# Kernel optimization log

Hardware: AMD Instinct MI355X
Metric: run time of the kernel (lower is better)

The kernel has to match this reference:

```python
import jax, jax.numpy as jnp
import numpy as np

N_NODES = 50000
N_EDGES = 800000
D = 128


def setup_inputs() -> dict:
    key = jax.random.key(0)
    ks = jax.random.split(key, 8)
    h = jax.random.normal(ks[0], (N_NODES, D), dtype=jnp.float32)
    src = jax.random.randint(ks[1], (N_EDGES,), 0, N_NODES, dtype=jnp.int64)
    dst = jax.random.randint(ks[2], (N_EDGES,), 0, N_NODES, dtype=jnp.int64)
    # Glorot-ish init for the three GraphConv weights
    scale = 1.0 / np.sqrt(D)
    W0 = jax.random.normal(ks[3], (D, D), dtype=jnp.float32) * scale
    W1 = jax.random.normal(ks[4], (D, D), dtype=jnp.float32) * scale
    W2 = jax.random.normal(ks[5], (D, D), dtype=jnp.float32) * scale
    b0 = jnp.zeros((D,), dtype=jnp.float32)
    b1 = jnp.zeros((D,), dtype=jnp.float32)
    b2 = jnp.zeros((D,), dtype=jnp.float32)
    return {"h": h, "src": src, "dst": dst, "W0": W0, "b0": b0,
            "W1": W1, "b1": b1, "W2": W2, "b2": b2}


def _graph_conv(x, src, dst, W, b, n_nodes):
    """DGL GraphConv, norm='both', activation=ReLU.
    in_feats == out_feats -> aggregate first, then matmul W."""
    ones = jnp.ones_like(src, dtype=x.dtype)
    out_deg = jnp.clip(jax.ops.segment_sum(ones, src, num_segments=n_nodes), 1.0)
    in_deg = jnp.clip(jax.ops.segment_sum(ones, dst, num_segments=n_nodes), 1.0)
    x = x * (out_deg ** -0.5)[:, None]          # src-side normalization
    m = jax.ops.segment_sum(x[src], dst, num_segments=n_nodes)  # sparse aggregation
    m = m * (in_deg ** -0.5)[:, None]           # dst-side normalization
    return jax.nn.relu(m @ W + b)


def reference(h, src, dst, W0, b0, W1, b1, W2, b2):
    n = h.shape[0]
    h = _graph_conv(h, src, dst, W0, b0, n)
    h = _graph_conv(h, src, dst, W1, b1, n)
    h = _graph_conv(h, src, dst, W2, b2, n)
    return h
```

## Files before the change

### kernel.cpp

```cpp
#include <hip/hip_runtime.h>

#define N_NODES 50000
#define N_EDGES 800000
#define D 128
#define CAP 48
#define MS_STRIDE 132
#define QNODES 12500
#define QWORDS (QNODES / 4)
#define HISTB 1024
#define EPB (N_EDGES / 256)
#define HWORDS (N_NODES / 4)
#define FILLB ((N_EDGES + 255) / 256)
#define REDB ((HWORDS + 255) / 256)

typedef __attribute__((ext_vector_type(4))) float f32x4;
typedef __attribute__((ext_vector_type(8))) short s16x8;

__device__ inline unsigned short f32_to_bf16_rtne(float f) {
    union { float f; unsigned u; } c; c.f = f;
    unsigned u = c.u;
    u += 0x7FFF + ((u >> 16) & 1);
    return (unsigned short)(u >> 16);
}
__device__ inline float bf16_to_f32(unsigned short h) {
    union { unsigned u; float f; } c; c.u = ((unsigned)h) << 16;
    return c.f;
}
__device__ inline unsigned pack_bf2(float a, float b) {
    return (unsigned)f32_to_bf16_rtne(a) | ((unsigned)f32_to_bf16_rtne(b) << 16);
}
__device__ inline void unpack_bf2(unsigned u, float& a, float& b) {
    union { unsigned u; float f; } c0, c1;
    c0.u = u << 16; c1.u = u & 0xFFFF0000u;
    a = c0.f; b = c1.f;
}
__device__ inline void acc_uint4(uint4 v, float* a) {
    float f0, f1;
    unpack_bf2(v.x, f0, f1); a[0] += f0; a[1] += f1;
    unpack_bf2(v.y, f0, f1); a[2] += f0; a[3] += f1;
    unpack_bf2(v.z, f0, f1); a[4] += f0; a[5] += f1;
    unpack_bf2(v.w, f0, f1); a[6] += f0; a[7] += f1;
}


__global__ __launch_bounds__(256) void build_all(const int* __restrict__ src,
                                                 const int* __restrict__ dst,
                                                 int* __restrict__ cursor,
                                                 unsigned* __restrict__ partial,
                                                 int* __restrict__ slots) {
    __shared__ unsigned hist[QWORDS];
    int b = blockIdx.x;
    if (b < HISTB) {
        int q = b >> 8, p = b & 255;
        int n0 = q * QNODES;
        for (int i = threadIdx.x; i < QWORDS; i += 256) hist[i] = 0;
        __syncthreads();
        int e0 = p * EPB;
        for (int i = threadIdx.x; i < EPB; i += 256) {
            int s = src[e0 + i];
            unsigned r = (unsigned)(s - n0);
            if (r < (unsigned)QNODES) atomicAdd(&hist[r >> 2], 1u << ((r & 3) * 8));
        }
        __syncthreads();
        unsigned* dstp = partial + (size_t)b * QWORDS;
        for (int i = threadIdx.x; i < QWORDS; i += 256) dstp[i] = hist[i];
    } else {
        int e = (b - HISTB) * 256 + threadIdx.x;
        if (e < N_EDGES) {
            int d = dst[e], s = src[e];
            int pos = atomicAdd(&cursor[d], 1);
            if (pos < CAP) slots[d * CAP + pos] = s;
        }
    }
}


__global__ __launch_bounds__(256) void mid_reduce_pack(const unsigned* __restrict__ partial,
                                                       float* __restrict__ s_out,
                                                       const float* __restrict__ W0,
                                                       const float* __restrict__ W1,
                                                       const float* __restrict__ W2,
                                                       s16x8* __restrict__ wpk) {
    int blk = blockIdx.x;
    if (blk < REDB) {
        int w = blk * 256 + threadIdx.x;
        if (w >= HWORDS) return;
        int q = w / QWORDS, wq = w - q * QWORDS;
        const unsigned* base = partial + (size_t)(q * 256) * QWORDS + wq;
        int c0 = 0, c1 = 0, c2 = 0, c3 = 0;
        for (int p = 0; p < 256; p++) {
            unsigned v = base[(size_t)p * QWORDS];
            c0 += v & 255; c1 += (v >> 8) & 255; c2 += (v >> 16) & 255; c3 += v >> 24;
        }
        float4 so;
        so.x = rsqrtf(fmaxf((float)c0, 1.0f));
        so.y = rsqrtf(fmaxf((float)c1, 1.0f));
        so.z = rsqrtf(fmaxf((float)c2, 1.0f));
        so.w = rsqrtf(fmaxf((float)c3, 1.0f));
        ((float4*)s_out)[w] = so;
    } else {
        int wid = (blk - REDB) * 4 + (threadIdx.x >> 6);
        if (wid >= 96) return;
        int lane = threadIdx.x & 63;
        int layer = wid / 32, rem = wid % 32;
        int ct = rem >> 2, ks = rem & 3;
        const float* W = (layer == 0) ? W0 : (layer == 1) ? W1 : W2;
        int col = ct * 16 + (lane & 15);
        int k0  = ks * 32 + (lane >> 4) * 8;
        s16x8 hi, lo;
#pragma unroll
        for (int j = 0; j < 8; j++) {
            float w = W[(k0 + j) * D + col];
            unsigned short h = f32_to_bf16_rtne(w);
            hi[j] = (short)h;
            lo[j] = (short)f32_to_bf16_rtne(w - bf16_to_f32(h));
        }
        int idx = layer * 4096 + (ct * 4 + ks) * 64 + lane;
        wpk[idx]        = hi;
        wpk[idx + 2048] = lo;
    }
}


__global__ __launch_bounds__(256) void hconv(const float4* __restrict__ h,
                                             const float* __restrict__ s_out,
                                             uint2* __restrict__ hbA,
                                             uint2* __restrict__ hbB) {
    int gid = blockIdx.x * 256 + threadIdx.x;
    const int total = N_NODES * 32;
    if (gid < total) {
        float so = s_out[gid >> 5];
        float4 v = h[gid];
        hbA[gid] = make_uint2(pack_bf2(so * v.x, so * v.y), pack_bf2(so * v.z, so * v.w));
    } else if (gid < total + 32) {
        hbA[total + (gid - total)] = make_uint2(0u, 0u);
    } else if (gid < total + 64) {
        hbB[total + (gid - total - 32)] = make_uint2(0u, 0u);
    }
}


__global__ __launch_bounds__(256) void fused_layer(const uint4* __restrict__ x,
                                                   const int* __restrict__ slots,
                                                   const int* __restrict__ deg,
                                                   const s16x8* __restrict__ wpk,
                                                   const float* __restrict__ bias,
                                                   const float* __restrict__ s_out,
                                                   float* __restrict__ outf,
                                                   unsigned short* __restrict__ outb) {
    __shared__ float mS[16 * MS_STRIDE];
    int tid = threadIdx.x;
    int row0 = blockIdx.x * 16;

    {
        int nloc = tid >> 4;
        int l    = tid & 15;
        int node = row0 + nloc;
        int dgraw = deg[node];
        int dg = min(dgraw, CAP);
        int base = node * CAP;
        int idx0 = (l      < dg) ? slots[base + l]      : N_NODES;
        int idx1 = (16 + l < dg) ? slots[base + 16 + l] : N_NODES;
        int idx2 = (32 + l < dg) ? slots[base + 32 + l] : N_NODES;

        float a[8];
#pragma unroll
        for (int j = 0; j < 8; j++) a[j] = 0.f;

        int nr = (dg + 7) >> 3;
        for (int r = 0; r < nr; r++) {
            int c = r >> 1;
            int v = (c == 0) ? idx0 : ((c == 1) ? idx1 : idx2);
            int k = (r & 1) * 8;
            int s0 = __shfl(v, k + 0, 16), s1 = __shfl(v, k + 1, 16);
            int s2 = __shfl(v, k + 2, 16), s3 = __shfl(v, k + 3, 16);
            int s4 = __shfl(v, k + 4, 16), s5 = __shfl(v, k + 5, 16);
            int s6 = __shfl(v, k + 6, 16), s7 = __shfl(v, k + 7, 16);
            uint4 g0 = x[s0 * 16 + l];
            uint4 g1 = x[s1 * 16 + l];
            uint4 g2 = x[s2 * 16 + l];
            uint4 g3 = x[s3 * 16 + l];
            uint4 g4 = x[s4 * 16 + l];
            uint4 g5 = x[s5 * 16 + l];
            uint4 g6 = x[s6 * 16 + l];
            uint4 g7 = x[s7 * 16 + l];
            acc_uint4(g0, a); acc_uint4(g1, a); acc_uint4(g2, a); acc_uint4(g3, a);
            acc_uint4(g4, a); acc_uint4(g5, a); acc_uint4(g6, a); acc_uint4(g7, a);
        }
        float si = rsqrtf(fmaxf((float)dgraw, 1.0f));
        float* dp = &mS[nloc * MS_STRIDE + l * 8];
#pragma unroll
        for (int j = 0; j < 8; j++) dp[j] = a[j] * si;
    }
    __syncthreads();

    int wv = tid >> 6;
    int lane = tid & 63;
    int arow = lane & 15, aq = lane >> 4;
    int ct0 = wv * 2, ct1 = ct0 + 1;
    f32x4 acc0 = (f32x4)0.f, acc1 = (f32x4)0.f;

#pragma unroll
    for (int ks = 0; ks < 4; ks++) {
        const float* ap = &mS[arow * MS_STRIDE + ks * 32 + aq * 8];
        s16x8 ahi, alo;
#pragma unroll
        for (int j = 0; j < 8; j++) {
            float av = ap[j];
            unsigned short hh = f32_to_bf16_rtne(av);
            ahi[j] = (short)hh;
            alo[j] = (short)f32_to_bf16_rtne(av - bf16_to_f32(hh));
        }
        int idx0 = (ct0 * 4 + ks) * 64 + lane;
        int idx1 = (ct1 * 4 + ks) * 64 + lane;
        s16x8 b0h = wpk[idx0], b0l = wpk[idx0 + 2048];
        s16x8 b1h = wpk[idx1], b1l = wpk[idx1 + 2048];
        acc0 = __builtin_amdgcn_mfma_f32_16x16x32_bf16(ahi, b0h, acc0, 0, 0, 0);
        acc0 = __builtin_amdgcn_mfma_f32_16x16x32_bf16(alo, b0h, acc0, 0, 0, 0);
        acc0 = __builtin_amdgcn_mfma_f32_16x16x32_bf16(ahi, b0l, acc0, 0, 0, 0);
        acc1 = __builtin_amdgcn_mfma_f32_16x16x32_bf16(ahi, b1h, acc1, 0, 0, 0);
        acc1 = __builtin_amdgcn_mfma_f32_16x16x32_bf16(alo, b1h, acc1, 0, 0, 0);
        acc1 = __builtin_amdgcn_mfma_f32_16x16x32_bf16(ahi, b1l, acc1, 0, 0, 0);
    }

    int crow0 = aq * 4;
    float so4[4];
    if (outb) {
#pragma unroll
        for (int r = 0; r < 4; r++) so4[r] = s_out[row0 + crow0 + r];
    }
    int colA = ct0 * 16 + arow, colB = ct1 * 16 + arow;
    float bA = bias[colA], bB = bias[colB];
#pragma unroll
    for (int r = 0; r < 4; r++) {
        size_t rowoff = (size_t)(row0 + crow0 + r) * D;
        float vA = fmaxf(acc0[r] + bA, 0.f);
        float vB = fmaxf(acc1[r] + bB, 0.f);
        if (outf) { outf[rowoff + colA] = vA; outf[rowoff + colB] = vB; }
        if (outb) {
            outb[rowoff + colA] = f32_to_bf16_rtne(so4[r] * vA);
            outb[rowoff + colB] = f32_to_bf16_rtne(so4[r] * vB);
        }
    }
}


extern "C" void kernel_launch(void* const* d_in, const int* in_sizes, int n_in,
                              void* d_out, int out_size, void* d_ws, size_t ws_size,
                              hipStream_t stream) {
    const float* h  = (const float*)d_in[0];
    const int*  src = (const int*)d_in[1];
    const int*  dst = (const int*)d_in[2];
    const float* W0 = (const float*)d_in[3];
    const float* b0 = (const float*)d_in[4];
    const float* W1 = (const float*)d_in[5];
    const float* b1 = (const float*)d_in[6];
    const float* W2 = (const float*)d_in[7];
    const float* b2 = (const float*)d_in[8];
    float* out = (float*)d_out;

    char* w = (char*)d_ws;
    auto carve = [&](size_t bytes) -> void* {
        void* p = (void*)w;
        w += (bytes + 255) & ~(size_t)255;
        return p;
    };
    int*      cursor  = (int*)carve(N_NODES * sizeof(int));
    float*    s_out   = (float*)carve(N_NODES * sizeof(float));
    int*      slots   = (int*)carve((size_t)N_NODES * CAP * sizeof(int));
    unsigned* partial = (unsigned*)carve((size_t)HISTB * QWORDS * sizeof(unsigned));
    unsigned short* actA = (unsigned short*)carve((size_t)(N_NODES + 1) * D * 2);
    unsigned short* actB = (unsigned short*)carve((size_t)(N_NODES + 1) * D * 2);
    s16x8*    wpk     = (s16x8*)carve(3 * 4096 * sizeof(s16x8));

    hipMemsetAsync(cursor, 0, N_NODES * sizeof(int), stream);
    build_all<<<HISTB + FILLB, 256, 0, stream>>>(src, dst, cursor, partial, slots);
    mid_reduce_pack<<<REDB + 24, 256, 0, stream>>>(partial, s_out, W0, W1, W2, wpk);
    hconv<<<(N_NODES * 32 + 64 + 255) / 256, 256, 0, stream>>>((const float4*)h, s_out,
                                                               (uint2*)actA, (uint2*)actB);

    const int GRID = N_NODES / 16;

    fused_layer<<<GRID, 256, 0, stream>>>((const uint4*)actA, slots, cursor,
                                          wpk, b0, s_out, nullptr, actB);
    fused_layer<<<GRID, 256, 0, stream>>>((const uint4*)actB, slots, cursor,
                                          wpk + 4096, b1, s_out, nullptr, actA);
    fused_layer<<<GRID, 256, 0, stream>>>((const uint4*)actA, slots, cursor,
                                          wpk + 8192, b2, s_out, out, nullptr);
}
```

Before: 263.3 us.

## Replace partial-histogram degree pass with range-partitioned global atomics and 16-bit slots

Out-degree counting no longer builds per-block shared-memory byte histograms written to a large partial buffer and reduced in a second pass. Instead, one fill kernel walks edge chunks once per node range and uses global atomics for both out-degree and the CSR-like slot fill. The separate reduction step is replaced by a simple per-node rsqrt pass. Neighbor slots are also stored as 16-bit indices, which is valid because the node count fits in 16 bits, halving index traffic in the gather layers. In exchange, src and dst are re-read once per range, and the degree counting now depends on global atomic throughput.

```diff
diff --git a/kernel.cpp b/kernel.cpp
--- a/kernel.cpp
+++ b/kernel.cpp
@@ -5,13 +5,14 @@
 #define D 128
 #define CAP 48
 #define MS_STRIDE 132
-#define QNODES 12500
-#define QWORDS (QNODES / 4)
-#define HISTB 1024
-#define EPB (N_EDGES / 256)
-#define HWORDS (N_NODES / 4)
-#define FILLB ((N_EDGES + 255) / 256)
-#define REDB ((HWORDS + 255) / 256)
+
+#define NPART 625
+#define EPB   (N_EDGES / NPART)
+#define NRANGE 8
+#define RNODES (N_NODES / NRANGE)
+#define FILLGRID (NPART * NRANGE)
+
+#define SBLK ((N_NODES + 255) / 256)
 
 typedef __attribute__((ext_vector_type(4))) float f32x4;
 typedef __attribute__((ext_vector_type(8))) short s16x8;
@@ -43,63 +44,42 @@
 }
 
 
-__global__ __launch_bounds__(256) void build_all(const int* __restrict__ src,
-                                                 const int* __restrict__ dst,
-                                                 int* __restrict__ cursor,
-                                                 unsigned* __restrict__ partial,
-                                                 int* __restrict__ slots) {
-    __shared__ unsigned hist[QWORDS];
+__global__ __launch_bounds__(256) void build_fill(const int* __restrict__ src,
+                                                  const int* __restrict__ dst,
+                                                  int* __restrict__ cursor,
+                                                  int* __restrict__ odeg,
+                                                  unsigned short* __restrict__ slots) {
     int b = blockIdx.x;
-    if (b < HISTB) {
-        int q = b >> 8, p = b & 255;
-        int n0 = q * QNODES;
-        for (int i = threadIdx.x; i < QWORDS; i += 256) hist[i] = 0;
-        __syncthreads();
-        int e0 = p * EPB;
-        for (int i = threadIdx.x; i < EPB; i += 256) {
-            int s = src[e0 + i];
-            unsigned r = (unsigned)(s - n0);
-            if (r < (unsigned)QNODES) atomicAdd(&hist[r >> 2], 1u << ((r & 3) * 8));
-        }
-        __syncthreads();
-        unsigned* dstp = partial + (size_t)b * QWORDS;
-        for (int i = threadIdx.x; i < QWORDS; i += 256) dstp[i] = hist[i];
+    int r = b & (NRANGE - 1);
+    int p = b >> 3;
+    int n0 = r * RNODES;
+    int e0 = p * EPB;
+    for (int i = threadIdx.x; i < EPB; i += 256) {
+        int e = e0 + i;
+        int s = src[e];
+        int d = dst[e];
+        if ((unsigned)(s - n0) < (unsigned)RNODES)
+            atomicAdd(&odeg[s], 1);
+        if ((unsigned)(d - n0) < (unsigned)RNODES) {
+            int pos = atomicAdd(&cursor[d], 1);
+            if (pos < CAP) slots[d * CAP + pos] = (unsigned short)s;
+        }
+    }
+}
+
+
+__global__ __launch_bounds__(256) void mid_pack(const int* __restrict__ odeg,
+                                                float* __restrict__ s_out,
+                                                const float* __restrict__ W0,
+                                                const float* __restrict__ W1,
+                                                const float* __restrict__ W2,
+                                                s16x8* __restrict__ wpk) {
+    int blk = blockIdx.x;
+    if (blk < SBLK) {
+        int i = blk * 256 + threadIdx.x;
+        if (i < N_NODES) s_out[i] = rsqrtf(fmaxf((float)odeg[i], 1.0f));
     } else {
-        int e = (b - HISTB) * 256 + threadIdx.x;
-        if (e < N_EDGES) {
-            int d = dst[e], s = src[e];
-            int pos = atomicAdd(&cursor[d], 1);
-            if (pos < CAP) slots[d * CAP + pos] = s;
-        }
-    }
-}
-
-
-__global__ __launch_bounds__(256) void mid_reduce_pack(const unsigned* __restrict__ partial,
-                                                       float* __restrict__ s_out,
-                                                       const float* __restrict__ W0,
-                                                       const float* __restrict__ W1,
-                                                       const float* __restrict__ W2,
-                                                       s16x8* __restrict__ wpk) {
-    int blk = blockIdx.x;
-    if (blk < REDB) {
-        int w = blk * 256 + threadIdx.x;
-        if (w >= HWORDS) return;
-        int q = w / QWORDS, wq = w - q * QWORDS;
-        const unsigned* base = partial + (size_t)(q * 256) * QWORDS + wq;
-        int c0 = 0, c1 = 0, c2 = 0, c3 = 0;
-        for (int p = 0; p < 256; p++) {
-            unsigned v = base[(size_t)p * QWORDS];
-            c0 += v & 255; c1 += (v >> 8) & 255; c2 += (v >> 16) & 255; c3 += v >> 24;
-        }
-        float4 so;
-        so.x = rsqrtf(fmaxf((float)c0, 1.0f));
-        so.y = rsqrtf(fmaxf((float)c1, 1.0f));
-        so.z = rsqrtf(fmaxf((float)c2, 1.0f));
-        so.w = rsqrtf(fmaxf((float)c3, 1.0f));
-        ((float4*)s_out)[w] = so;
-    } else {
-        int wid = (blk - REDB) * 4 + (threadIdx.x >> 6);
+        int wid = (blk - SBLK) * 4 + (threadIdx.x >> 6);
         if (wid >= 96) return;
         int lane = threadIdx.x & 63;
         int layer = wid / 32, rem = wid % 32;
@@ -141,7 +121,7 @@
 
 
 __global__ __launch_bounds__(256) void fused_layer(const uint4* __restrict__ x,
-                                                   const int* __restrict__ slots,
+                                                   const unsigned short* __restrict__ slots,
                                                    const int* __restrict__ deg,
                                                    const s16x8* __restrict__ wpk,
                                                    const float* __restrict__ bias,
@@ -159,9 +139,9 @@
         int dgraw = deg[node];
         int dg = min(dgraw, CAP);
         int base = node * CAP;
-        int idx0 = (l      < dg) ? slots[base + l]      : N_NODES;
-        int idx1 = (16 + l < dg) ? slots[base + 16 + l] : N_NODES;
-        int idx2 = (32 + l < dg) ? slots[base + 32 + l] : N_NODES;
+        int idx0 = (l      < dg) ? (int)slots[base + l]      : N_NODES;
+        int idx1 = (16 + l < dg) ? (int)slots[base + 16 + l] : N_NODES;
+        int idx2 = (32 + l < dg) ? (int)slots[base + 32 + l] : N_NODES;
 
         float a[8];
 #pragma unroll
@@ -265,17 +245,17 @@
         w += (bytes + 255) & ~(size_t)255;
         return p;
     };
-    int*      cursor  = (int*)carve(N_NODES * sizeof(int));
+    int*      cursor  = (int*)carve(2 * N_NODES * sizeof(int));
+    int*      odeg    = cursor + N_NODES;
     float*    s_out   = (float*)carve(N_NODES * sizeof(float));
-    int*      slots   = (int*)carve((size_t)N_NODES * CAP * sizeof(int));
-    unsigned* partial = (unsigned*)carve((size_t)HISTB * QWORDS * sizeof(unsigned));
-    unsigned short* actA = (unsigned short*)carve((size_t)(N_NODES + 1) * D * 2);
-    unsigned short* actB = (unsigned short*)carve((size_t)(N_NODES + 1) * D * 2);
+    unsigned short* slots = (unsigned short*)carve((size_t)N_NODES * CAP * sizeof(unsigned short));
+    unsigned short* actA  = (unsigned short*)carve((size_t)(N_NODES + 1) * D * 2);
+    unsigned short* actB  = (unsigned short*)carve((size_t)(N_NODES + 1) * D * 2);
     s16x8*    wpk     = (s16x8*)carve(3 * 4096 * sizeof(s16x8));
 
-    hipMemsetAsync(cursor, 0, N_NODES * sizeof(int), stream);
-    build_all<<<HISTB + FILLB, 256, 0, stream>>>(src, dst, cursor, partial, slots);
-    mid_reduce_pack<<<REDB + 24, 256, 0, stream>>>(partial, s_out, W0, W1, W2, wpk);
+    hipMemsetAsync(cursor, 0, 2 * N_NODES * sizeof(int), stream);
+    build_fill<<<FILLGRID, 256, 0, stream>>>(src, dst, cursor, odeg, slots);
+    mid_pack<<<SBLK + 24, 256, 0, stream>>>(odeg, s_out, W0, W1, W2, wpk);
     hconv<<<(N_NODES * 32 + 64 + 255) / 256, 256, 0, stream>>>((const float4*)h, s_out,
                                                                (uint2*)actA, (uint2*)actB);
 
```

After: 262.2 us. Within noise of the previous version (-0.4%).
